# Optimization experiments

Measured on AMD Instinct MI355X. Metric: run time of the kernel, lower is better.

Reference implementation:

```python
import jax, jax.numpy as jnp
import numpy as np

K = 3
EPS = 1e-8


def setup_inputs() -> dict:
    key = jax.random.key(0)
    k1, k2, k3 = jax.random.split(key, 3)
    N, M, C = 16384, 32768, 128
    return {
        "source_points": jax.random.normal(k1, (N, 3), dtype=jnp.float32),
        "source_features": jax.random.normal(k2, (N, C), dtype=jnp.float32),
        "target_points": jax.random.normal(k3, (M, 3), dtype=jnp.float32),
    }


def reference(source_points, source_features, target_points):
    # Squared euclidean distances [M, N] via the expanded form
    # ||t - s||^2 = ||t||^2 - 2 t.s + ||s||^2 (same math, avoids [M,N,3] temp)
    t2 = jnp.sum(target_points * target_points, axis=-1, keepdims=True)   # [M,1]
    s2 = jnp.sum(source_points * source_points, axis=-1)                  # [N]
    cross = jnp.einsum("md,nd->mn", target_points, source_points)        # [M,N]
    dists = t2 - 2.0 * cross + s2[None, :]                                # [M,N]

    k = min(K, source_points.shape[0])
    # smallest-k distances -> top_k on negated values
    neg_d, knn_idx = jax.lax.top_k(-dists, k)                             # [M,k]
    knn_dists = -neg_d

    weights = 1.0 / (knn_dists + EPS)                                     # inverse-distance weights
    weights = weights / jnp.sum(weights, axis=1, keepdims=True)           # [M,k]

    knn_features = source_features[knn_idx]                               # [M,k,C] gather
    return jnp.sum(knn_features * weights[..., None], axis=1)             # [M,C]
```

## Files before the change

kernel.cpp:

```cpp
#include <hip/hip_runtime.h>
#include <math.h>
#include <stdint.h>

#define EPS 1e-8f
#define FMAXV 3.402823466e38f

#define GD2 64
#define NC2 (GD2 * GD2)
#define BLO (-6.0f)
#define INVCS (5.3333335f)
#define MARGIN 2e-4f

__device__ __forceinline__ int mcell(float v) {
    int c = (int)floorf((v - BLO) * INVCS);
    return min(max(c, 0), GD2 - 1);
}
__device__ __forceinline__ int skey2(float x, float y) {
    return mcell(y) * GD2 + mcell(x);
}
__device__ __forceinline__ int qkey2(float x, float y) {
    int r = mcell(y), c = mcell(x);
    return r * GD2 + ((r & 1) ? (GD2 - 1 - c) : c);
}
__device__ __forceinline__ float finf() { return __uint_as_float(0x7f800000u); }

__device__ __forceinline__ unsigned key_hi(float d) {
    unsigned b = __float_as_uint(d);
    return (b & 0x80000000u) ? ~b : (b | 0x80000000u);
}
__device__ __forceinline__ float key_d(unsigned long long k) {
    unsigned h = (unsigned)(k >> 32);
    unsigned b = (h & 0x80000000u) ? (h & 0x7fffffffu) : ~h;
    return __uint_as_float(b);
}
__device__ __forceinline__ unsigned long long shfl_xor_u64(unsigned long long v, int m) {
    int lo = __shfl_xor((int)(unsigned)(v & 0xffffffffu), m, 64);
    int hi = __shfl_xor((int)(unsigned)(v >> 32), m, 64);
    return ((unsigned long long)(unsigned)hi << 32) | (unsigned)lo;
}
__device__ __forceinline__ void insert3k(unsigned long long k,
        unsigned long long& k0, unsigned long long& k1, unsigned long long& k2) {
    const bool c0 = k < k0, c1 = k < k1, c2 = k < k2;
    k2 = c1 ? k1 : (c2 ? k : k2);
    k1 = c0 ? k0 : (c1 ? k : k1);
    k0 = c0 ? k : k0;
}
__device__ __forceinline__ void insert3f(float d, float& d0, float& d1, float& d2) {
    const bool c0 = d < d0, c1 = d < d1, c2 = d < d2;
    d2 = c1 ? d1 : (c2 ? d : d2);
    d1 = c0 ? d0 : (c1 ? d : d1);
    d0 = c0 ? d : d0;
}
__device__ __forceinline__ void merge3f(float b0, float b1, float b2,
                                        float& a0, float& a1, float& a2) {
    float r0 = fminf(a0, b0);
    float r1 = fminf(fminf(a1, b1), fmaxf(a0, b0));
    float r2 = fminf(fminf(a2, b2), fminf(fmaxf(a1, b0), fmaxf(a0, b1)));
    a0 = r0; a1 = r1; a2 = r2;
}
__device__ __forceinline__ unsigned long long umin64(unsigned long long a, unsigned long long b) { return a < b ? a : b; }
__device__ __forceinline__ unsigned long long umax64(unsigned long long a, unsigned long long b) { return a < b ? b : a; }
__device__ __forceinline__ void merge3k(unsigned long long b0, unsigned long long b1, unsigned long long b2,
        unsigned long long& a0, unsigned long long& a1, unsigned long long& a2) {
    unsigned long long r0 = umin64(a0, b0);
    unsigned long long r1 = umin64(umin64(a1, b1), umax64(a0, b0));
    unsigned long long r2 = umin64(umin64(a2, b2), umin64(umax64(a1, b0), umax64(a0, b1)));
    a0 = r0; a1 = r1; a2 = r2;
}

__global__ void k_hist2D(const float* __restrict__ sp, int N,
                         const float* __restrict__ tp, int M,
                         int* __restrict__ scnt, int* __restrict__ qcnt) {
    int i = blockIdx.x * 256 + threadIdx.x;
    if (i < N) {
        atomicAdd(&scnt[skey2(sp[3 * i], sp[3 * i + 1])], 1);
    } else if (i < N + M) {
        int j = i - N;
        atomicAdd(&qcnt[qkey2(tp[3 * j], tp[3 * j + 1])], 1);
    }
}

__global__ __launch_bounds__(1024) void k_scan4k(int* __restrict__ scnt, int* __restrict__ qcnt,
                                                 int* __restrict__ soffs, int* __restrict__ qoffs) {
    int* cnt  = blockIdx.x ? qcnt : scnt;
    int* offs = blockIdx.x ? qoffs : soffs;
    __shared__ int sh[1024];
    const int t = threadIdx.x;
    int4 v = ((const int4*)cnt)[t];
    int s = v.x + v.y + v.z + v.w;
    sh[t] = s;
    __syncthreads();
    for (int o = 1; o < 1024; o <<= 1) {
        int u = (t >= o) ? sh[t - o] : 0;
        __syncthreads();
        sh[t] += u;
        __syncthreads();
    }
    int base = sh[t] - s;
    int4 e = make_int4(base, base + v.x, base + v.x + v.y, base + v.x + v.y + v.z);
    ((int4*)offs)[t] = e;
    ((int4*)cnt)[t]  = e;
    if (t == 1023) offs[NC2] = base + s;
}

__global__ void k_scat2D(const float* __restrict__ sp, int N,
                         const float* __restrict__ tp, int M,
                         int* __restrict__ scur, float4* __restrict__ spts, int* __restrict__ sidx,
                         int* __restrict__ qcur, float4* __restrict__ qpts) {
    int i = blockIdx.x * 256 + threadIdx.x;
    if (i < N) {
        float x = sp[3 * i], y = sp[3 * i + 1], z = sp[3 * i + 2];
        int pos = atomicAdd(&scur[skey2(x, y)], 1);
        float s2 = __fadd_rn(__fadd_rn(__fmul_rn(x, x), __fmul_rn(y, y)), __fmul_rn(z, z));
        spts[pos] = make_float4(-2.f * x, -2.f * y, -2.f * z, s2);
        sidx[pos] = i;
    } else if (i < N + M) {
        int j = i - N;
        float x = tp[3 * j], y = tp[3 * j + 1], z = tp[3 * j + 2];
        int pos = atomicAdd(&qcur[qkey2(x, y)], 1);
        qpts[pos] = make_float4(x, y, z, __int_as_float(j));
    }
}

#define SCORE_ONLY(pp) ({                                                     \
    float _a = fmaf((pp).z, qz, fmaf((pp).y, qy, __fmul_rn((pp).x, qx)));     \
    __fadd_rn(__fadd_rn(t2, _a), (pp).w); })

__global__ __launch_bounds__(256) void k_knn_w2(
        const float4* __restrict__ spts, const int* __restrict__ sidx,
        const int* __restrict__ soffs, const float4* __restrict__ qpts,
        const float* __restrict__ feat, float* __restrict__ out,
        int N, int M, int C) {
    const int lane = threadIdx.x & 63;
    const int wave = __builtin_amdgcn_readfirstlane(threadIdx.x >> 6);
    const int qid  = blockIdx.x * 4 + wave;
    if (qid >= M) return;

    float4 qp = qpts[qid];
    const float qx = qp.x, qy = qp.y, qz = qp.z;
    const int orig = __float_as_int(qp.w);
    const float t2 = __fadd_rn(__fadd_rn(__fmul_rn(qx, qx), __fmul_rn(qy, qy)),
                               __fmul_rn(qz, qz));

    const int ck = mcell(qy) * GD2 + mcell(qx);
    const int ca = soffs[ck], cb = soffs[ck + 1];
    const int ctr = (ca + cb) >> 1;
    const int p0 = min(max(ctr - 128, 0), N - 256);

    float d0 = FMAXV, d1 = FMAXV, d2 = FMAXV;
    #pragma unroll
    for (int s = 0; s < 4; ++s) {
        float4 pt = spts[p0 + lane + s * 64];
        insert3f(SCORE_ONLY(pt), d0, d1, d2);
    }
    #pragma unroll
    for (int r = 1; r < 64; r <<= 1) {
        float e0 = __shfl_xor(d0, r, 64);
        float e1 = __shfl_xor(d1, r, 64);
        float e2 = __shfl_xor(d2, r, 64);
        merge3f(e0, e1, e2, d0, d1, d2);
    }
    const float w = sqrtf(__fadd_rn(d2, MARGIN));

    const int rlo = mcell(qy - w), rhi = mcell(qy + w);
    const int clo = mcell(qx - w), chi = mcell(qx + w);

    unsigned long long k0 = ~0ULL, k1 = ~0ULL, k2 = ~0ULL;
    for (int r = rlo; r <= rhi; ++r) {
        const int b = r << 6;
        const int S0 = soffs[b + clo], S1 = soffs[b + chi + 1];
        for (int p = S0 + lane; p < S1; p += 64) {
            float4 pt = spts[p];
            int    j  = sidx[p];
            float  d  = SCORE_ONLY(pt);
            insert3k(((unsigned long long)key_hi(d) << 32) | (unsigned)j, k0, k1, k2);
        }
    }
    #pragma unroll
    for (int r = 1; r < 64; r <<= 1) {
        unsigned long long m0 = shfl_xor_u64(k0, r);
        unsigned long long m1 = shfl_xor_u64(k1, r);
        unsigned long long m2 = shfl_xor_u64(k2, r);
        merge3k(m0, m1, m2, k0, k1, k2);
    }

    const float b0 = key_d(k0), b1 = key_d(k1), b2 = key_d(k2);
    const float w0r = __fdiv_rn(1.f, __fadd_rn(b0, EPS));
    const float w1r = __fdiv_rn(1.f, __fadd_rn(b1, EPS));
    const float w2r = __fdiv_rn(1.f, __fadd_rn(b2, EPS));
    const float sum = __fadd_rn(__fadd_rn(w0r, w1r), w2r);
    const float w0 = __fdiv_rn(w0r, sum);
    const float w1 = __fdiv_rn(w1r, sum);
    const float w2 = __fdiv_rn(w2r, sum);
    const int j0 = (int)(unsigned)(k0 & 0xffffffffu);
    const int j1 = (int)(unsigned)(k1 & 0xffffffffu);
    const int j2 = (int)(unsigned)(k2 & 0xffffffffu);

    const float2* f0 = (const float2*)(feat + (size_t)j0 * C);
    const float2* f1 = (const float2*)(feat + (size_t)j1 * C);
    const float2* f2 = (const float2*)(feat + (size_t)j2 * C);
    float2* o = (float2*)(out + (size_t)orig * C);
    const int nc2 = C >> 1;
    for (int cc = lane; cc < nc2; cc += 64) {
        float2 a = f0[cc], b = f1[cc], d = f2[cc];
        o[cc] = make_float2(w0 * a.x + w1 * b.x + w2 * d.x,
                            w0 * a.y + w1 * b.y + w2 * d.y);
    }
}

#define NW 16
__global__ void knn_preproc(const float* __restrict__ sp, float4* __restrict__ sp4, int N) {
    int j = blockIdx.x * blockDim.x + threadIdx.x;
    if (j < N) {
        float x = sp[3 * j + 0], y = sp[3 * j + 1], z = sp[3 * j + 2];
        float s2 = __fadd_rn(__fadd_rn(__fmul_rn(x, x), __fmul_rn(y, y)), __fmul_rn(z, z));
        sp4[j] = make_float4(-2.f * x, -2.f * y, -2.f * z, s2);
    }
}
__device__ __forceinline__ void insert3_bl(float d, int j,
                                           float& d0, float& d1, float& d2,
                                           int& i0, int& i1, int& i2) {
    const bool c0 = d < d0, c1 = d < d1, c2 = d < d2;
    const float nd2 = c1 ? d1 : (c2 ? d : d2);
    const int   ni2 = c1 ? i1 : (c2 ? j : i2);
    const float nd1 = c0 ? d0 : (c1 ? d : d1);
    const int   ni1 = c0 ? i0 : (c1 ? j : i1);
    const float nd0 = c0 ? d : d0;
    const int   ni0 = c0 ? j : i0;
    d0 = nd0; d1 = nd1; d2 = nd2;
    i0 = ni0; i1 = ni1; i2 = ni2;
}
#define SCORE_INSERT(p, jv) do {                                          \
    float _a = fmaf((p).z, tz, fmaf((p).y, ty, __fmul_rn((p).x, tx)));    \
    float _d = __fadd_rn(__fadd_rn(t2, _a), (p).w);                       \
    if (__any(_d < d2))                                                   \
        insert3_bl(_d, (jv), d0, d1, d2, i0, i1, i2);                     \
} while (0)
__global__ __launch_bounds__(1024, 8) void knn_dense(
    const float4* __restrict__ sp4, const float* __restrict__ feat,
    const float* __restrict__ tp, float* __restrict__ out,
    int N, int M, int C) {
    __shared__ float s_d[NW][3][64];
    __shared__ int   s_i[NW][3][64];
    __shared__ float s_w[3][64];
    __shared__ int   s_j[3][64];
    const int tid  = threadIdx.x;
    const int lane = tid & 63;
    const int wave = __builtin_amdgcn_readfirstlane(tid >> 6);
    const int mbase = blockIdx.x * 64;
    const int m = mbase + lane;
    float tx = 0.f, ty = 0.f, tz = 0.f;
    if (m < M) { tx = tp[3 * m + 0]; ty = tp[3 * m + 1]; tz = tp[3 * m + 2]; }
    const float t2 = __fadd_rn(__fadd_rn(__fmul_rn(tx, tx), __fmul_rn(ty, ty)),
                               __fmul_rn(tz, tz));
    float d0 = FMAXV, d1 = FMAXV, d2 = FMAXV;
    int   i0 = 0,     i1 = 0,     i2 = 0;
    const int chunk = (N + NW - 1) / NW;
    const int jbeg = wave * chunk;
    const int jend = min(jbeg + chunk, N);
    int j = jbeg;
    for (; j + 8 <= jend; j += 8) {
        float4 p0 = sp4[j + 0], p1 = sp4[j + 1], p2 = sp4[j + 2], p3 = sp4[j + 3];
        float4 p4 = sp4[j + 4], p5 = sp4[j + 5], p6 = sp4[j + 6], p7 = sp4[j + 7];
        SCORE_INSERT(p0, j + 0); SCORE_INSERT(p1, j + 1);
        SCORE_INSERT(p2, j + 2); SCORE_INSERT(p3, j + 3);
        SCORE_INSERT(p4, j + 4); SCORE_INSERT(p5, j + 5);
        SCORE_INSERT(p6, j + 6); SCORE_INSERT(p7, j + 7);
    }
    for (; j < jend; ++j) { float4 p = sp4[j]; SCORE_INSERT(p, j); }
    s_d[wave][0][lane] = d0; s_d[wave][1][lane] = d1; s_d[wave][2][lane] = d2;
    s_i[wave][0][lane] = i0; s_i[wave][1][lane] = i1; s_i[wave][2][lane] = i2;
    __syncthreads();
    if (wave == 0) {
        float b0 = FMAXV, b1 = FMAXV, b2 = FMAXV;
        int   j0 = 0,     j1 = 0,     j2 = 0;
        #pragma unroll
        for (int w = 0; w < NW; ++w)
            #pragma unroll
            for (int k = 0; k < 3; ++k)
                insert3_bl(s_d[w][k][lane], s_i[w][k][lane], b0, b1, b2, j0, j1, j2);
        float w0 = __fdiv_rn(1.f, __fadd_rn(b0, EPS));
        float w1 = __fdiv_rn(1.f, __fadd_rn(b1, EPS));
        float w2 = __fdiv_rn(1.f, __fadd_rn(b2, EPS));
        float sum = __fadd_rn(__fadd_rn(w0, w1), w2);
        s_w[0][lane] = __fdiv_rn(w0, sum);
        s_w[1][lane] = __fdiv_rn(w1, sum);
        s_w[2][lane] = __fdiv_rn(w2, sum);
        s_j[0][lane] = j0; s_j[1][lane] = j1; s_j[2][lane] = j2;
    }
    __syncthreads();
    const int tm = tid >> 4;
    const int qq = tid & 15;
    const int gm = mbase + tm;
    if (gm < M) {
        const int nv = C >> 6;
        const float w0 = s_w[0][tm], w1 = s_w[1][tm], w2 = s_w[2][tm];
        const float4* f0 = (const float4*)(feat + (size_t)s_j[0][tm] * C) + qq * nv;
        const float4* f1 = (const float4*)(feat + (size_t)s_j[1][tm] * C) + qq * nv;
        const float4* f2 = (const float4*)(feat + (size_t)s_j[2][tm] * C) + qq * nv;
        float4* o = (float4*)(out + (size_t)gm * C) + qq * nv;
        for (int r = 0; r < nv; ++r) {
            float4 a = f0[r], b = f1[r], c = f2[r];
            float4 v;
            v.x = w0 * a.x + w1 * b.x + w2 * c.x;
            v.y = w0 * a.y + w1 * b.y + w2 * c.y;
            v.z = w0 * a.z + w1 * b.z + w2 * c.z;
            v.w = w0 * a.w + w1 * b.w + w2 * c.w;
            o[r] = v;
        }
    }
}

static inline size_t align256(size_t x) { return (x + 255) & ~(size_t)255; }

extern "C" void kernel_launch(void* const* d_in, const int* in_sizes, int n_in,
                              void* d_out, int out_size, void* d_ws, size_t ws_size,
                              hipStream_t stream) {
    const float* sp   = (const float*)d_in[0];
    const float* feat = (const float*)d_in[1];
    const float* tp   = (const float*)d_in[2];
    float* out = (float*)d_out;

    const int N = in_sizes[0] / 3;
    const int C = in_sizes[1] / N;
    const int M = in_sizes[2] / 3;

    size_t oScnt  = 0;
    size_t oQcnt  = oScnt + (size_t)NC2 * 4;
    size_t oSoffs = align256(oQcnt + (size_t)NC2 * 4);
    size_t oQoffs = align256(oSoffs + (size_t)(NC2 + 1) * 4);
    size_t oSpts  = align256(oQoffs + (size_t)(NC2 + 1) * 4);
    size_t oSidx  = align256(oSpts + (size_t)N * 16);
    size_t oQpts  = align256(oSidx + (size_t)N * 4);
    size_t need   = oQpts + (size_t)M * 16;

    if (ws_size >= need && (C & 1) == 0 && N >= 256) {
        char* ws = (char*)d_ws;
        int*    scnt  = (int*)(ws + oScnt);
        int*    qcnt  = (int*)(ws + oQcnt);
        int*    soffs = (int*)(ws + oSoffs);
        int*    qoffs = (int*)(ws + oQoffs);
        float4* spts  = (float4*)(ws + oSpts);
        int*    sidxp = (int*)(ws + oSidx);
        float4* qpts  = (float4*)(ws + oQpts);

        hipMemsetAsync(scnt, 0, (size_t)2 * NC2 * 4, stream);
        int nmBlocks = (N + M + 255) / 256;
        k_hist2D<<<nmBlocks, 256, 0, stream>>>(sp, N, tp, M, scnt, qcnt);
        k_scan4k<<<2, 1024, 0, stream>>>(scnt, qcnt, soffs, qoffs);
        k_scat2D<<<nmBlocks, 256, 0, stream>>>(sp, N, tp, M, scnt, spts, sidxp, qcnt, qpts);
        k_knn_w2<<<(M + 3) / 4, 256, 0, stream>>>(spts, sidxp, soffs, qpts, feat, out, N, M, C);
    } else {
        float4* sp4 = (float4*)d_ws;
        knn_preproc<<<(N + 255) / 256, 256, 0, stream>>>(sp, sp4, N);
        knn_dense<<<(M + 63) / 64, 1024, 0, stream>>>(sp4, feat, tp, out, N, M, C);
    }
}
```

Baseline: 96.14 us.

## Reuse seed window top-3 and skip rescanning it; sparse ballot merge

The kNN kernel now computes exact top-3 keys (with indices) from the 256-point seed window via three wave-min reductions. The cell search then skips the seed range [p0,p1) so those points are not scored twice. The final merge only shuffles from lanes whose local top-3 changed, chosen with a ballot, in place of a full butterfly merge. Each wave also handles two queries sequentially to cut block count. The cost is more serial reductions per query and less parallelism per wave.

New measurement: 99.24 us, median of 5. 1.03x slower.

```diff
diff --git a/kernel.cpp b/kernel.cpp
--- a/kernel.cpp
+++ b/kernel.cpp
@@ -1,6 +1,8 @@
 #include <hip/hip_runtime.h>
 #include <math.h>
 #include <stdint.h>
+
+typedef unsigned long long u64;
 
 #define EPS 1e-8f
 #define FMAXV 3.402823466e38f
@@ -28,44 +30,34 @@
     unsigned b = __float_as_uint(d);
     return (b & 0x80000000u) ? ~b : (b | 0x80000000u);
 }
-__device__ __forceinline__ float key_d(unsigned long long k) {
+__device__ __forceinline__ float key_d(u64 k) {
     unsigned h = (unsigned)(k >> 32);
     unsigned b = (h & 0x80000000u) ? (h & 0x7fffffffu) : ~h;
     return __uint_as_float(b);
 }
-__device__ __forceinline__ unsigned long long shfl_xor_u64(unsigned long long v, int m) {
+__device__ __forceinline__ u64 shfl_xor_u64(u64 v, int m) {
     int lo = __shfl_xor((int)(unsigned)(v & 0xffffffffu), m, 64);
     int hi = __shfl_xor((int)(unsigned)(v >> 32), m, 64);
-    return ((unsigned long long)(unsigned)hi << 32) | (unsigned)lo;
-}
-__device__ __forceinline__ void insert3k(unsigned long long k,
-        unsigned long long& k0, unsigned long long& k1, unsigned long long& k2) {
+    return ((u64)(unsigned)hi << 32) | (unsigned)lo;
+}
+__device__ __forceinline__ u64 shfl_u64_from(u64 v, int l) {
+    int lo = __shfl((int)(unsigned)(v & 0xffffffffu), l, 64);
+    int hi = __shfl((int)(unsigned)(v >> 32), l, 64);
+    return ((u64)(unsigned)hi << 32) | (unsigned)lo;
+}
+__device__ __forceinline__ void insert3k(u64 k, u64& k0, u64& k1, u64& k2) {
     const bool c0 = k < k0, c1 = k < k1, c2 = k < k2;
     k2 = c1 ? k1 : (c2 ? k : k2);
     k1 = c0 ? k0 : (c1 ? k : k1);
     k0 = c0 ? k : k0;
 }
-__device__ __forceinline__ void insert3f(float d, float& d0, float& d1, float& d2) {
-    const bool c0 = d < d0, c1 = d < d1, c2 = d < d2;
-    d2 = c1 ? d1 : (c2 ? d : d2);
-    d1 = c0 ? d0 : (c1 ? d : d1);
-    d0 = c0 ? d : d0;
-}
-__device__ __forceinline__ void merge3f(float b0, float b1, float b2,
-                                        float& a0, float& a1, float& a2) {
-    float r0 = fminf(a0, b0);
-    float r1 = fminf(fminf(a1, b1), fmaxf(a0, b0));
-    float r2 = fminf(fminf(a2, b2), fminf(fmaxf(a1, b0), fmaxf(a0, b1)));
-    a0 = r0; a1 = r1; a2 = r2;
-}
-__device__ __forceinline__ unsigned long long umin64(unsigned long long a, unsigned long long b) { return a < b ? a : b; }
-__device__ __forceinline__ unsigned long long umax64(unsigned long long a, unsigned long long b) { return a < b ? b : a; }
-__device__ __forceinline__ void merge3k(unsigned long long b0, unsigned long long b1, unsigned long long b2,
-        unsigned long long& a0, unsigned long long& a1, unsigned long long& a2) {
-    unsigned long long r0 = umin64(a0, b0);
-    unsigned long long r1 = umin64(umin64(a1, b1), umax64(a0, b0));
-    unsigned long long r2 = umin64(umin64(a2, b2), umin64(umax64(a1, b0), umax64(a0, b1)));
-    a0 = r0; a1 = r1; a2 = r2;
+__device__ __forceinline__ u64 wave_min_u64(u64 v) {
+    #pragma unroll
+    for (int r = 1; r < 64; r <<= 1) {
+        u64 o = shfl_xor_u64(v, r);
+        v = (o < v) ? o : v;
+    }
+    return v;
 }
 
 __global__ void k_hist2D(const float* __restrict__ sp, int N,
@@ -126,85 +118,106 @@
     float _a = fmaf((pp).z, qz, fmaf((pp).y, qy, __fmul_rn((pp).x, qx)));     \
     __fadd_rn(__fadd_rn(t2, _a), (pp).w); })
 
-__global__ __launch_bounds__(256) void k_knn_w2(
+#define QPW 2
+
+__global__ __launch_bounds__(256) void k_knn_w3(
         const float4* __restrict__ spts, const int* __restrict__ sidx,
         const int* __restrict__ soffs, const float4* __restrict__ qpts,
         const float* __restrict__ feat, float* __restrict__ out,
         int N, int M, int C) {
     const int lane = threadIdx.x & 63;
     const int wave = __builtin_amdgcn_readfirstlane(threadIdx.x >> 6);
-    const int qid  = blockIdx.x * 4 + wave;
-    if (qid >= M) return;
-
-    float4 qp = qpts[qid];
-    const float qx = qp.x, qy = qp.y, qz = qp.z;
-    const int orig = __float_as_int(qp.w);
-    const float t2 = __fadd_rn(__fadd_rn(__fmul_rn(qx, qx), __fmul_rn(qy, qy)),
-                               __fmul_rn(qz, qz));
-
-    const int ck = mcell(qy) * GD2 + mcell(qx);
-    const int ca = soffs[ck], cb = soffs[ck + 1];
-    const int ctr = (ca + cb) >> 1;
-    const int p0 = min(max(ctr - 128, 0), N - 256);
-
-    float d0 = FMAXV, d1 = FMAXV, d2 = FMAXV;
+    const int qbase = (blockIdx.x * 4 + wave) * QPW;
+
     #pragma unroll
-    for (int s = 0; s < 4; ++s) {
-        float4 pt = spts[p0 + lane + s * 64];
-        insert3f(SCORE_ONLY(pt), d0, d1, d2);
-    }
-    #pragma unroll
-    for (int r = 1; r < 64; r <<= 1) {
-        float e0 = __shfl_xor(d0, r, 64);
-        float e1 = __shfl_xor(d1, r, 64);
-        float e2 = __shfl_xor(d2, r, 64);
-        merge3f(e0, e1, e2, d0, d1, d2);
-    }
-    const float w = sqrtf(__fadd_rn(d2, MARGIN));
-
-    const int rlo = mcell(qy - w), rhi = mcell(qy + w);
-    const int clo = mcell(qx - w), chi = mcell(qx + w);
-
-    unsigned long long k0 = ~0ULL, k1 = ~0ULL, k2 = ~0ULL;
-    for (int r = rlo; r <= rhi; ++r) {
-        const int b = r << 6;
-        const int S0 = soffs[b + clo], S1 = soffs[b + chi + 1];
-        for (int p = S0 + lane; p < S1; p += 64) {
+    for (int qi = 0; qi < QPW; ++qi) {
+        const int qid = qbase + qi;
+        if (qid >= M) break;
+        float4 qp = qpts[qid];
+        const float qx = qp.x, qy = qp.y, qz = qp.z;
+        const int orig = __float_as_int(qp.w);
+        const float t2 = __fadd_rn(__fadd_rn(__fmul_rn(qx, qx), __fmul_rn(qy, qy)),
+                                   __fmul_rn(qz, qz));
+
+        const int ck = mcell(qy) * GD2 + mcell(qx);
+        const int ca = soffs[ck], cb = soffs[ck + 1];
+        const int ctr = (ca + cb) >> 1;
+        const int p0 = min(max(ctr - 128, 0), N - 256);
+        const int p1 = p0 + 256;
+
+        u64 k0 = ~0ULL, k1 = ~0ULL, k2 = ~0ULL;
+        #pragma unroll
+        for (int s = 0; s < 4; ++s) {
+            const int p = p0 + lane + s * 64;
             float4 pt = spts[p];
-            int    j  = sidx[p];
-            float  d  = SCORE_ONLY(pt);
-            insert3k(((unsigned long long)key_hi(d) << 32) | (unsigned)j, k0, k1, k2);
-        }
-    }
-    #pragma unroll
-    for (int r = 1; r < 64; r <<= 1) {
-        unsigned long long m0 = shfl_xor_u64(k0, r);
-        unsigned long long m1 = shfl_xor_u64(k1, r);
-        unsigned long long m2 = shfl_xor_u64(k2, r);
-        merge3k(m0, m1, m2, k0, k1, k2);
-    }
-
-    const float b0 = key_d(k0), b1 = key_d(k1), b2 = key_d(k2);
-    const float w0r = __fdiv_rn(1.f, __fadd_rn(b0, EPS));
-    const float w1r = __fdiv_rn(1.f, __fadd_rn(b1, EPS));
-    const float w2r = __fdiv_rn(1.f, __fadd_rn(b2, EPS));
-    const float sum = __fadd_rn(__fadd_rn(w0r, w1r), w2r);
-    const float w0 = __fdiv_rn(w0r, sum);
-    const float w1 = __fdiv_rn(w1r, sum);
-    const float w2 = __fdiv_rn(w2r, sum);
-    const int j0 = (int)(unsigned)(k0 & 0xffffffffu);
-    const int j1 = (int)(unsigned)(k1 & 0xffffffffu);
-    const int j2 = (int)(unsigned)(k2 & 0xffffffffu);
-
-    const float2* f0 = (const float2*)(feat + (size_t)j0 * C);
-    const float2* f1 = (const float2*)(feat + (size_t)j1 * C);
-    const float2* f2 = (const float2*)(feat + (size_t)j2 * C);
-    float2* o = (float2*)(out + (size_t)orig * C);
-    const int nc2 = C >> 1;
-    for (int cc = lane; cc < nc2; cc += 64) {
-        float2 a = f0[cc], b = f1[cc], d = f2[cc];
-        o[cc] = make_float2(w0 * a.x + w1 * b.x + w2 * d.x,
-                            w0 * a.y + w1 * b.y + w2 * d.y);
+            int j = sidx[p];
+            float d = SCORE_ONLY(pt);
+            insert3k(((u64)key_hi(d) << 32) | (unsigned)j, k0, k1, k2);
+        }
+        u64 T0 = wave_min_u64(k0);
+        { bool h = (k0 == T0); k0 = h ? k1 : k0; k1 = h ? k2 : k1; k2 = h ? ~0ULL : k2; }
+        u64 T1 = wave_min_u64(k0);
+        { bool h = (k0 == T1); k0 = h ? k1 : k0; k1 = h ? k2 : k1; }
+        u64 T2 = wave_min_u64(k0);
+
+        const float b3 = key_d(T2);
+        const float w = sqrtf(__fadd_rn(b3, MARGIN));
+        const int rlo = mcell(qy - w), rhi = mcell(qy + w);
+        const int clo = mcell(qx - w), chi = mcell(qx + w);
+
+        u64 a0 = T0, a1 = T1, a2 = T2;
+        for (int r = rlo; r <= rhi; ++r) {
+            const int b = r << 6;
+            const int A = soffs[b + clo], B = soffs[b + chi + 1];
+            const int Lend = min(B, p0);
+            for (int p = A + lane; p < Lend; p += 64) {
+                float4 pt = spts[p]; int j = sidx[p];
+                float d = SCORE_ONLY(pt);
+                insert3k(((u64)key_hi(d) << 32) | (unsigned)j, a0, a1, a2);
+            }
+            const int Rbeg = max(A, p1);
+            for (int p = Rbeg + lane; p < B; p += 64) {
+                float4 pt = spts[p]; int j = sidx[p];
+                float d = SCORE_ONLY(pt);
+                insert3k(((u64)key_hi(d) << 32) | (unsigned)j, a0, a1, a2);
+            }
+        }
+        const bool changed = (a0 != T0) || (a1 != T1) || (a2 != T2);
+        u64 mb = __ballot(changed);
+        const u64 S0 = T0, S1 = T1, S2 = T2;
+        while (mb) {
+            int l = __builtin_ctzll(mb);
+            mb &= mb - 1;
+            u64 m0 = shfl_u64_from(a0, l);
+            u64 m1 = shfl_u64_from(a1, l);
+            u64 m2 = shfl_u64_from(a2, l);
+            if (m0 != S0 && m0 != S1 && m0 != S2) insert3k(m0, T0, T1, T2);
+            if (m1 != S0 && m1 != S1 && m1 != S2) insert3k(m1, T0, T1, T2);
+            if (m2 != S0 && m2 != S1 && m2 != S2) insert3k(m2, T0, T1, T2);
+        }
+
+        const float d0 = key_d(T0), d1 = key_d(T1), d2 = key_d(T2);
+        const float w0r = __fdiv_rn(1.f, __fadd_rn(d0, EPS));
+        const float w1r = __fdiv_rn(1.f, __fadd_rn(d1, EPS));
+        const float w2r = __fdiv_rn(1.f, __fadd_rn(d2, EPS));
+        const float sum = __fadd_rn(__fadd_rn(w0r, w1r), w2r);
+        const float w0 = __fdiv_rn(w0r, sum);
+        const float w1 = __fdiv_rn(w1r, sum);
+        const float w2 = __fdiv_rn(w2r, sum);
+        const int j0 = (int)(unsigned)(T0 & 0xffffffffu);
+        const int j1 = (int)(unsigned)(T1 & 0xffffffffu);
+        const int j2 = (int)(unsigned)(T2 & 0xffffffffu);
+
+        const float2* f0 = (const float2*)(feat + (size_t)j0 * C);
+        const float2* f1 = (const float2*)(feat + (size_t)j1 * C);
+        const float2* f2 = (const float2*)(feat + (size_t)j2 * C);
+        float2* o = (float2*)(out + (size_t)orig * C);
+        const int nc2 = C >> 1;
+        for (int cc = lane; cc < nc2; cc += 64) {
+            float2 a = f0[cc], b = f1[cc], d = f2[cc];
+            o[cc] = make_float2(w0 * a.x + w1 * b.x + w2 * d.x,
+                                w0 * a.y + w1 * b.y + w2 * d.y);
+        }
     }
 }
 
@@ -349,7 +362,8 @@
         k_hist2D<<<nmBlocks, 256, 0, stream>>>(sp, N, tp, M, scnt, qcnt);
         k_scan4k<<<2, 1024, 0, stream>>>(scnt, qcnt, soffs, qoffs);
         k_scat2D<<<nmBlocks, 256, 0, stream>>>(sp, N, tp, M, scnt, spts, sidxp, qcnt, qpts);
-        k_knn_w2<<<(M + 3) / 4, 256, 0, stream>>>(spts, sidxp, soffs, qpts, feat, out, N, M, C);
+        int qblocks = (M + 4 * QPW - 1) / (4 * QPW);
+        k_knn_w3<<<qblocks, 256, 0, stream>>>(spts, sidxp, soffs, qpts, feat, out, N, M, C);
     } else {
         float4* sp4 = (float4*)d_ws;
         knn_preproc<<<(N + 255) / 256, 256, 0, stream>>>(sp, sp4, N);
```
